# Optimization experiments

Hardware: AMD Instinct MI355X
Metric: run time of the kernel (lower is better)

Reference implementation:

```python
import jax, jax.numpy as jnp
import numpy as np

C_IN = 12      # total channels (rgb-noised + hidden)
C_NOISE = 3    # noise-prediction channels
HID = 128      # rule-MLP hidden size
PERC = 48      # perception channels (depthwise, 48/12 = 4 filters per channel)
TDIM = 256     # sinusoidal time-embedding dim


def setup_inputs() -> dict:
    key = jax.random.key(0)
    ks = jax.random.split(key, 12)
    B, H, W = 16, 256, 256
    x = jax.random.normal(ks[0], (B, C_NOISE, H, W), jnp.float32)
    hidden_channels = jax.random.normal(ks[1], (B, C_IN - C_NOISE, H, W), jnp.float32)
    t = jax.random.randint(ks[2], (B,), 0, 1000)
    # depthwise 3x3 perceive conv: torch weight shape [out=48, in/groups=1, 3, 3]
    w_perceive = jax.random.normal(ks[3], (PERC, 1, 3, 3), jnp.float32) * 0.1
    b_perceive = jax.random.normal(ks[4], (PERC,), jnp.float32) * 0.01
    # 1x1 convs of the rule network, stored as [out, in]
    w1 = jax.random.normal(ks[5], (HID, PERC), jnp.float32) * 0.1
    b1 = jax.random.normal(ks[6], (HID,), jnp.float32) * 0.01
    w2 = jax.random.normal(ks[7], (HID, HID), jnp.float32) * 0.05
    b2 = jax.random.normal(ks[8], (HID,), jnp.float32) * 0.01
    # conv3 is zero-initialized in the original; random here for test coverage
    w3 = jax.random.normal(ks[9], (C_IN, HID), jnp.float32) * 0.05
    # time embedding Linear(256 -> c_noise)
    w_time = jax.random.normal(ks[10], (C_NOISE, TDIM), jnp.float32) * 0.1
    b_time = jax.random.normal(ks[11], (C_NOISE,), jnp.float32) * 0.01
    return dict(x=x, hidden_channels=hidden_channels, t=t,
                w_perceive=w_perceive, b_perceive=b_perceive,
                w1=w1, b1=b1, w2=w2, b2=b2, w3=w3,
                w_time=w_time, b_time=b_time)


def _pos_encoding(t, channels):
    # t: [B] int -> [B, channels] sinusoidal embedding (torch repeat-then-scale layout)
    inv_freq = 1.0 / (10000.0 ** (jnp.arange(0, channels, 2, dtype=jnp.float32) / channels))
    ang = t.astype(jnp.float32)[:, None] * inv_freq  # [B, channels//2]
    return jnp.concatenate([jnp.sin(ang), jnp.cos(ang)], axis=-1)


def reference(x, hidden_channels, t, w_perceive, b_perceive, w1, b1, w2, b2, w3, w_time, b_time):
    # concat noised channels with hidden state channels -> [B, 12, H, W]
    xf = jnp.concatenate([x, hidden_channels], axis=1)
    # depthwise 3x3 conv, 'same' padding, groups = C_IN
    perc = jax.lax.conv_general_dilated(
        xf, w_perceive, window_strides=(1, 1), padding='SAME',
        feature_group_count=C_IN,
        dimension_numbers=('NCHW', 'OIHW', 'NCHW')) + b_perceive[None, :, None, None]
    # rule network: three 1x1 convs (pointwise MLP) with ReLUs
    h = jax.nn.relu(jnp.einsum('bchw,oc->bohw', perc, w1) + b1[None, :, None, None])
    h = jax.nn.relu(jnp.einsum('bchw,oc->bohw', h, w2) + b2[None, :, None, None])
    out = jnp.einsum('bchw,oc->bohw', h, w3)  # no bias
    # time embedding: sinusoidal -> SiLU -> Linear -> broadcast over H, W
    pe = _pos_encoding(t, TDIM)                       # [B, 256]
    emb = jax.nn.silu(pe) @ w_time.T + b_time         # [B, 3]
    noise_prediction = out[:, :C_NOISE] + emb[:, :, None, None]
    hidden_out = out[:, C_NOISE:]
    return (hidden_out, noise_prediction)
```

## Files before the change

### kernel.cpp

```cpp
#include <hip/hip_runtime.h>


#define ACT_S 136
#define NOISE_BASE 9437184

#define WSF_OFF 13312
#define WSF_BP 0
#define WSF_B1 48
#define WSF_B2 176
#define WSF_WP 304
#define WSF_EMB 736

typedef short bf16x8 __attribute__((ext_vector_type(8)));
typedef float f32x4 __attribute__((ext_vector_type(4)));

__device__ __forceinline__ short f2bf(float f) {
    union { float f; unsigned u; } cv; cv.f = f;
    unsigned r = cv.u + 0x7FFFu + ((cv.u >> 16) & 1u);
    return (short)(r >> 16);
}
__device__ __forceinline__ unsigned pk2bf(float f0, float f1) {
    union { float f; unsigned u; } a, b; a.f = f0; b.f = f1;
    return __builtin_amdgcn_perm(b.u + 0x8000u, a.u + 0x8000u, 0x07060302u);
}

__global__ void prep_emb_kernel(const float* __restrict__ wpg, const float* __restrict__ bpg,
                                const float* __restrict__ w1g, const float* __restrict__ b1g,
                                const float* __restrict__ w2g, const float* __restrict__ b2g,
                                const float* __restrict__ w3g,
                                const int* __restrict__ t,
                                const float* __restrict__ wt, const float* __restrict__ bt,
                                short* __restrict__ wsb, float* __restrict__ wsf)
{
    if (blockIdx.x < 107) {
        int i = blockIdx.x * 256 + threadIdx.x;
        if (i < 8192) {
            int o = i >> 6, c = i & 63;
            wsb[i] = (c < 48) ? f2bf(w1g[o * 48 + c]) : (short)0;
        } else if (i < 24576) {
            wsb[i] = f2bf(w2g[i - 8192]);
        } else if (i < 26624) {
            int k = i - 24576;
            wsb[i] = (k < 1536) ? f2bf(w3g[k]) : (short)0;
        } else if (i < 26672) {
            wsf[WSF_BP + (i - 26624)] = bpg[i - 26624];
        } else if (i < 26800) {
            wsf[WSF_B1 + (i - 26672)] = b1g[i - 26672];
        } else if (i < 26928) {
            wsf[WSF_B2 + (i - 26800)] = b2g[i - 26800];
        } else if (i < 27360) {
            wsf[WSF_WP + (i - 26928)] = wpg[i - 26928];
        }
        return;
    }
    int b = blockIdx.x - 107;
    int lane = threadIdx.x;
    if (lane >= 64) return;
    float tv = (float)t[b];
    float s0 = 0.f, s1 = 0.f, s2 = 0.f;
    const float LOG1E4 = 9.210340371976184f;
    #pragma unroll
    for (int ii = 0; ii < 2; ++ii) {
        int i = lane + ii * 64;
        float invf = __expf(-LOG1E4 * (float)i * (1.0f / 128.0f));
        float ang = tv * invf;
        float sn = sinf(ang), cs = cosf(ang);
        float ss = sn / (1.0f + __expf(-sn));
        float sc = cs / (1.0f + __expf(-cs));
        s0 += ss * wt[0 * 256 + i] + sc * wt[0 * 256 + i + 128];
        s1 += ss * wt[1 * 256 + i] + sc * wt[1 * 256 + i + 128];
        s2 += ss * wt[2 * 256 + i] + sc * wt[2 * 256 + i + 128];
    }
    #pragma unroll
    for (int off = 32; off; off >>= 1) {
        s0 += __shfl_down(s0, off);
        s1 += __shfl_down(s1, off);
        s2 += __shfl_down(s2, off);
    }
    if (lane == 0) {
        wsf[WSF_EMB + b * 3 + 0] = s0 + bt[0];
        wsf[WSF_EMB + b * 3 + 1] = s1 + bt[1];
        wsf[WSF_EMB + b * 3 + 2] = s2 + bt[2];
    }
}

__global__ __launch_bounds__(256, 3) void canet_main(
    const float* __restrict__ xg,
    const float* __restrict__ hg,
    const short* __restrict__ wsb,
    const float* __restrict__ wsf,
    float* __restrict__ outg)
{
    __shared__ __align__(16) short bufA[64 * ACT_S];
    __shared__ __align__(16) short h1S[64 * ACT_S];
    __shared__ __align__(16) float wp_s[48 * 12];
    __shared__ float bp_s[48];

    const int tid = threadIdx.x;
    const int b = blockIdx.x >> 8;
    const int y = blockIdx.x & 255;

    for (int i = tid; i < 576; i += 256) {
        int oc = i / 12, k = i % 12;
        wp_s[i] = (k < 9) ? wsf[WSF_WP + oc * 9 + k] : 0.0f;
    }
    if (tid < 48) bp_s[tid] = wsf[WSF_BP + tid];

    const int wv = tid >> 6;
    const int lane = tid & 63;
    const int m = lane & 15;
    const int q = lane >> 4;

    bf16x8 w1f[2][2], w2f[2][4], w3f[4];
    #pragma unroll
    for (int j = 0; j < 2; ++j) {
        int n = wv * 32 + j * 16 + m;
        #pragma unroll
        for (int ks = 0; ks < 2; ++ks)
            w1f[j][ks] = *(const bf16x8*)(wsb + n * 64 + ks * 32 + q * 8);
        #pragma unroll
        for (int ks = 0; ks < 4; ++ks)
            w2f[j][ks] = *(const bf16x8*)(wsb + 8192 + n * 128 + ks * 32 + q * 8);
    }
    #pragma unroll
    for (int ks = 0; ks < 4; ++ks)
        w3f[ks] = *(const bf16x8*)(wsb + 24576 + m * 128 + ks * 32 + q * 8);

    f32x4 b1v[2], b2v[2];
    #pragma unroll
    for (int j = 0; j < 2; ++j) {
        b1v[j] = *(const f32x4*)(wsf + WSF_B1 + wv * 32 + j * 16 + q * 4);
        b2v[j] = *(const f32x4*)(wsf + WSF_B2 + wv * 32 + j * 16 + q * 4);
    }
    const float embv = (m < 3) ? wsf[WSF_EMB + b * 3 + m] : 0.0f;

    const float* src3[3];
    #pragma unroll
    for (int i3 = 0; i3 < 3; ++i3) {
        int ic = 3 * q + i3;
        src3[i3] = (ic < 3) ? (xg + (((size_t)b * 3 + ic) << 16))
                            : (hg + (((size_t)b * 9 + (ic - 3)) << 16));
    }

    __syncthreads();

    for (int it = 0; it < 4; ++it) {
        const int x0 = it * 64;
        const int px = x0 + wv * 16 + m;

        {
            const int xm1 = px - (px > 0);
            const int xp1 = px + (px < 255);
            const bool okl = (px > 0), okr = (px < 255);
            short* prow = bufA + (wv * 16 + m) * ACT_S;
            const bool interior = (y >= 1) && (y <= 254);
            #pragma unroll
            for (int i3 = 0; i3 < 3; ++i3) {
                const float* s = src3[i3];
                float tap[9];
                if (interior) {
                    #pragma unroll
                    for (int ky = 0; ky < 3; ++ky) {
                        const float* rp = s + (y + ky - 1) * 256;
                        float c0 = rp[xm1], c1 = rp[px], c2 = rp[xp1];
                        tap[ky * 3 + 0] = okl ? c0 : 0.0f;
                        tap[ky * 3 + 1] = c1;
                        tap[ky * 3 + 2] = okr ? c2 : 0.0f;
                    }
                } else {
                    #pragma unroll
                    for (int ky = 0; ky < 3; ++ky) {
                        int yy = y + ky - 1;
                        bool yok = (yy >= 0) && (yy < 256);
                        const float* rp = s + (yok ? yy : y) * 256;
                        float c0 = rp[xm1], c1 = rp[px], c2 = rp[xp1];
                        tap[ky * 3 + 0] = (yok && okl) ? c0 : 0.0f;
                        tap[ky * 3 + 1] = yok ? c1 : 0.0f;
                        tap[ky * 3 + 2] = (yok && okr) ? c2 : 0.0f;
                    }
                }
                float v[4];
                #pragma unroll
                for (int r = 0; r < 4; ++r) {
                    int oc = 12 * q + 4 * i3 + r;
                    const float* wrow = &wp_s[oc * 12];
                    f32x4 w0 = *(const f32x4*)wrow;
                    f32x4 w1_ = *(const f32x4*)(wrow + 4);
                    float a = bp_s[oc];
                    a += w0[0] * tap[0] + w0[1] * tap[1] + w0[2] * tap[2] + w0[3] * tap[3];
                    a += w1_[0] * tap[4] + w1_[1] * tap[5] + w1_[2] * tap[6] + w1_[3] * tap[7];
                    a += wrow[8] * tap[8];
                    v[r] = a;
                }
                uint2 pk;
                pk.x = pk2bf(v[0], v[1]);
                pk.y = pk2bf(v[2], v[3]);
                *(uint2*)(prow + 12 * q + 4 * i3) = pk;
            }
            *(uint2*)(prow + 48 + 4 * q) = uint2{0u, 0u};
        }
        __syncthreads();

        #pragma unroll
        for (int nt = 0; nt < 4; ++nt) {
            f32x4 c0 = b1v[0], c1 = b1v[1];
            #pragma unroll
            for (int ks = 0; ks < 2; ++ks) {
                bf16x8 p = *(const bf16x8*)(bufA + (nt * 16 + m) * ACT_S + ks * 32 + q * 8);
                c0 = __builtin_amdgcn_mfma_f32_16x16x32_bf16(w1f[0][ks], p, c0, 0, 0, 0);
                c1 = __builtin_amdgcn_mfma_f32_16x16x32_bf16(w1f[1][ks], p, c1, 0, 0, 0);
            }
            short* drow = h1S + (nt * 16 + m) * ACT_S + wv * 32 + q * 4;
            uint2 pk;
            pk.x = pk2bf(fmaxf(c0[0], 0.f), fmaxf(c0[1], 0.f));
            pk.y = pk2bf(fmaxf(c0[2], 0.f), fmaxf(c0[3], 0.f));
            *(uint2*)drow = pk;
            pk.x = pk2bf(fmaxf(c1[0], 0.f), fmaxf(c1[1], 0.f));
            pk.y = pk2bf(fmaxf(c1[2], 0.f), fmaxf(c1[3], 0.f));
            *(uint2*)(drow + 16) = pk;
        }
        __syncthreads();

        #pragma unroll
        for (int nt = 0; nt < 4; ++nt) {
            f32x4 c0 = b2v[0], c1 = b2v[1];
            #pragma unroll
            for (int ks = 0; ks < 4; ++ks) {
                bf16x8 a = *(const bf16x8*)(h1S + (nt * 16 + m) * ACT_S + ks * 32 + q * 8);
                c0 = __builtin_amdgcn_mfma_f32_16x16x32_bf16(w2f[0][ks], a, c0, 0, 0, 0);
                c1 = __builtin_amdgcn_mfma_f32_16x16x32_bf16(w2f[1][ks], a, c1, 0, 0, 0);
            }
            short* drow = bufA + (nt * 16 + m) * ACT_S + wv * 32 + q * 4;
            uint2 pk;
            pk.x = pk2bf(fmaxf(c0[0], 0.f), fmaxf(c0[1], 0.f));
            pk.y = pk2bf(fmaxf(c0[2], 0.f), fmaxf(c0[3], 0.f));
            *(uint2*)drow = pk;
            pk.x = pk2bf(fmaxf(c1[0], 0.f), fmaxf(c1[1], 0.f));
            pk.y = pk2bf(fmaxf(c1[2], 0.f), fmaxf(c1[3], 0.f));
            *(uint2*)(drow + 16) = pk;
        }
        __syncthreads();

        {
            f32x4 acc = {0.f, 0.f, 0.f, 0.f};
            #pragma unroll
            for (int ks = 0; ks < 4; ++ks) {
                bf16x8 a = *(const bf16x8*)(bufA + (wv * 16 + m) * ACT_S + ks * 32 + q * 8);
                acc = __builtin_amdgcn_mfma_f32_16x16x32_bf16(a, w3f[ks], acc, 0, 0, 0);
            }
            if (m < 12) {
                int xx0 = x0 + wv * 16 + q * 4;
                size_t idx;
                if (m < 3) {
                    idx = (size_t)NOISE_BASE + (((size_t)b * 3 + m) << 16) + (size_t)y * 256 + xx0;
                } else {
                    idx = (((size_t)b * 9 + (m - 3)) << 16) + (size_t)y * 256 + xx0;
                }
                f32x4 vst = {acc[0] + embv, acc[1] + embv, acc[2] + embv, acc[3] + embv};
                *(f32x4*)(outg + idx) = vst;
            }
        }
        __syncthreads();
    }
}

extern "C" void kernel_launch(void* const* d_in, const int* in_sizes, int n_in,
                              void* d_out, int out_size, void* d_ws, size_t ws_size,
                              hipStream_t stream) {
    const float* xg  = (const float*)d_in[0];
    const float* hg  = (const float*)d_in[1];
    const int*   tg  = (const int*)  d_in[2];
    const float* wpg = (const float*)d_in[3];
    const float* bpg = (const float*)d_in[4];
    const float* w1g = (const float*)d_in[5];
    const float* b1g = (const float*)d_in[6];
    const float* w2g = (const float*)d_in[7];
    const float* b2g = (const float*)d_in[8];
    const float* w3g = (const float*)d_in[9];
    const float* wtg = (const float*)d_in[10];
    const float* btg = (const float*)d_in[11];
    float* outg = (float*)d_out;
    short* wsb  = (short*)d_ws;
    float* wsf  = (float*)d_ws + WSF_OFF;

    prep_emb_kernel<<<123, 256, 0, stream>>>(wpg, bpg, w1g, b1g, w2g, b2g, w3g,
                                             tg, wtg, btg, wsb, wsf);
    canet_main<<<4096, 256, 0, stream>>>(xg, hg, wsb, wsf, outg);
}
```

Baseline: 224.6 us.

## Move w3 and biases to LDS and transpose perceive weights to raise occupancy

Moves the w3 fragment and the two bias vectors from registers into shared memory, using an XOR-swizzled layout for w3, and raises launch bounds from 3 to 4 blocks per SM. The perceive weights are stored transposed (tap-major) so the depthwise conv reads one vector per tap covering four output channels. The aim is to cut VGPR pressure so more waves can hide global-load latency. The cost is extra LDS reads inside the MLP and output stages.

```diff
diff --git a/kernel.cpp b/kernel.cpp
--- a/kernel.cpp
+++ b/kernel.cpp
@@ -49,7 +49,9 @@
         } else if (i < 26928) {
             wsf[WSF_B2 + (i - 26800)] = b2g[i - 26800];
         } else if (i < 27360) {
-            wsf[WSF_WP + (i - 26928)] = wpg[i - 26928];
+            int idx = i - 26928;
+            int oc = idx / 9, k = idx % 9;
+            wsf[WSF_WP + k * 48 + oc] = wpg[idx];
         }
         return;
     }
@@ -84,7 +86,7 @@
     }
 }
 
-__global__ __launch_bounds__(256, 3) void canet_main(
+__global__ __launch_bounds__(256, 4) void canet_main(
     const float* __restrict__ xg,
     const float* __restrict__ hg,
     const short* __restrict__ wsb,
@@ -93,25 +95,29 @@
 {
     __shared__ __align__(16) short bufA[64 * ACT_S];
     __shared__ __align__(16) short h1S[64 * ACT_S];
-    __shared__ __align__(16) float wp_s[48 * 12];
-    __shared__ float bp_s[48];
+    __shared__ __align__(16) short w3_s[12 * 128];
+    __shared__ __align__(16) float wpT_s[9 * 48];
+    __shared__ __align__(16) float bias_s[256];
+    __shared__ __align__(16) float bp_s[48];
 
     const int tid = threadIdx.x;
     const int b = blockIdx.x >> 8;
     const int y = blockIdx.x & 255;
 
-    for (int i = tid; i < 576; i += 256) {
-        int oc = i / 12, k = i % 12;
-        wp_s[i] = (k < 9) ? wsf[WSF_WP + oc * 9 + k] : 0.0f;
-    }
+    for (int i = tid; i < 432; i += 256) wpT_s[i] = wsf[WSF_WP + i];
     if (tid < 48) bp_s[tid] = wsf[WSF_BP + tid];
+    bias_s[tid] = wsf[WSF_B1 + tid];
+    for (int i = tid; i < 1536; i += 256) {
+        int row = i >> 7, col = i & 127;
+        w3_s[(row << 7) + (col ^ ((row & 7) << 3))] = wsb[24576 + i];
+    }
 
     const int wv = tid >> 6;
     const int lane = tid & 63;
     const int m = lane & 15;
     const int q = lane >> 4;
 
-    bf16x8 w1f[2][2], w2f[2][4], w3f[4];
+    bf16x8 w1f[2][2], w2f[2][4];
     #pragma unroll
     for (int j = 0; j < 2; ++j) {
         int n = wv * 32 + j * 16 + m;
@@ -121,16 +127,6 @@
         #pragma unroll
         for (int ks = 0; ks < 4; ++ks)
             w2f[j][ks] = *(const bf16x8*)(wsb + 8192 + n * 128 + ks * 32 + q * 8);
-    }
-    #pragma unroll
-    for (int ks = 0; ks < 4; ++ks)
-        w3f[ks] = *(const bf16x8*)(wsb + 24576 + m * 128 + ks * 32 + q * 8);
-
-    f32x4 b1v[2], b2v[2];
-    #pragma unroll
-    for (int j = 0; j < 2; ++j) {
-        b1v[j] = *(const f32x4*)(wsf + WSF_B1 + wv * 32 + j * 16 + q * 4);
-        b2v[j] = *(const f32x4*)(wsf + WSF_B2 + wv * 32 + j * 16 + q * 4);
     }
     const float embv = (m < 3) ? wsf[WSF_EMB + b * 3 + m] : 0.0f;
 
@@ -141,6 +137,9 @@
         src3[i3] = (ic < 3) ? (xg + (((size_t)b * 3 + ic) << 16))
                             : (hg + (((size_t)b * 9 + (ic - 3)) << 16));
     }
+
+    const int mm = (m < 12) ? m : 11;
+    const int w3sw = (mm & 7) << 3;
 
     __syncthreads();
 
@@ -179,22 +178,17 @@
                         tap[ky * 3 + 2] = (yok && okr) ? c2 : 0.0f;
                     }
                 }
-                float v[4];
+                f32x4 a4 = *(const f32x4*)(bp_s + 12 * q + 4 * i3);
                 #pragma unroll
-                for (int r = 0; r < 4; ++r) {
-                    int oc = 12 * q + 4 * i3 + r;
-                    const float* wrow = &wp_s[oc * 12];
-                    f32x4 w0 = *(const f32x4*)wrow;
-                    f32x4 w1_ = *(const f32x4*)(wrow + 4);
-                    float a = bp_s[oc];
-                    a += w0[0] * tap[0] + w0[1] * tap[1] + w0[2] * tap[2] + w0[3] * tap[3];
-                    a += w1_[0] * tap[4] + w1_[1] * tap[5] + w1_[2] * tap[6] + w1_[3] * tap[7];
-                    a += wrow[8] * tap[8];
-                    v[r] = a;
+                for (int k = 0; k < 9; ++k) {
+                    f32x4 w4 = *(const f32x4*)(wpT_s + k * 48 + 12 * q + 4 * i3);
+                    float t = tap[k];
+                    a4[0] += w4[0] * t; a4[1] += w4[1] * t;
+                    a4[2] += w4[2] * t; a4[3] += w4[3] * t;
                 }
                 uint2 pk;
-                pk.x = pk2bf(v[0], v[1]);
-                pk.y = pk2bf(v[2], v[3]);
+                pk.x = pk2bf(a4[0], a4[1]);
+                pk.y = pk2bf(a4[2], a4[3]);
                 *(uint2*)(prow + 12 * q + 4 * i3) = pk;
             }
             *(uint2*)(prow + 48 + 4 * q) = uint2{0u, 0u};
@@ -203,7 +197,8 @@
 
         #pragma unroll
         for (int nt = 0; nt < 4; ++nt) {
-            f32x4 c0 = b1v[0], c1 = b1v[1];
+            f32x4 c0 = *(const f32x4*)(bias_s + wv * 32 + q * 4);
+            f32x4 c1 = *(const f32x4*)(bias_s + wv * 32 + 16 + q * 4);
             #pragma unroll
             for (int ks = 0; ks < 2; ++ks) {
                 bf16x8 p = *(const bf16x8*)(bufA + (nt * 16 + m) * ACT_S + ks * 32 + q * 8);
@@ -223,7 +218,8 @@
 
         #pragma unroll
         for (int nt = 0; nt < 4; ++nt) {
-            f32x4 c0 = b2v[0], c1 = b2v[1];
+            f32x4 c0 = *(const f32x4*)(bias_s + 128 + wv * 32 + q * 4);
+            f32x4 c1 = *(const f32x4*)(bias_s + 128 + wv * 32 + 16 + q * 4);
             #pragma unroll
             for (int ks = 0; ks < 4; ++ks) {
                 bf16x8 a = *(const bf16x8*)(h1S + (nt * 16 + m) * ACT_S + ks * 32 + q * 8);
@@ -246,7 +242,8 @@
             #pragma unroll
             for (int ks = 0; ks < 4; ++ks) {
                 bf16x8 a = *(const bf16x8*)(bufA + (wv * 16 + m) * ACT_S + ks * 32 + q * 8);
-                acc = __builtin_amdgcn_mfma_f32_16x16x32_bf16(a, w3f[ks], acc, 0, 0, 0);
+                bf16x8 w3k = *(const bf16x8*)(w3_s + (mm << 7) + ((ks * 32 + q * 8) ^ w3sw));
+                acc = __builtin_amdgcn_mfma_f32_16x16x32_bf16(a, w3k, acc, 0, 0, 0);
             }
             if (m < 12) {
                 int xx0 = x0 + wv * 16 + q * 4;
```

Result: no change. 228.0 us (+1.5%).
